# Kernel optimization log

Hardware: AMD Instinct MI355X
Metric: run time of the kernel (lower is better)

Reference implementation:

```python
import jax, jax.numpy as jnp
import numpy as np

B, L, D, H = 2, 2048, 1024, 16
HD = D // H


def setup_inputs() -> dict:
    key = jax.random.key(0)
    ks = jax.random.split(key, 8)
    x = jax.random.normal(ks[0], (B, L, D), dtype=jnp.float32)
    WQ = jax.random.normal(ks[1], (D, D), dtype=jnp.float32) * 0.02
    bQ = jnp.zeros((D,), dtype=jnp.float32)
    WK = jax.random.normal(ks[2], (D, D), dtype=jnp.float32) * 0.02
    bK = jnp.zeros((D,), dtype=jnp.float32)
    WV = jax.random.normal(ks[3], (D, D), dtype=jnp.float32) * 0.02
    bV = jnp.zeros((D,), dtype=jnp.float32)
    Wc = jax.random.normal(ks[4], (D, D), dtype=jnp.float32) * 0.02  # dense channel-mix matrix [d_out, d_in]
    return {"x": x, "WQ": WQ, "bQ": bQ, "WK": WK, "bK": bK, "WV": WV, "bV": bV, "Wc": Wc}


def reference(x, WQ, bQ, WK, bK, WV, bV, Wc):
    b, l, d = x.shape
    # --- TokenMixWeightGenerator (LOW_RANK): T = softmax(causal(Q K^T / sqrt(hd)))
    q = (x @ WQ.T + bQ).reshape(b, l, H, HD).transpose(0, 2, 1, 3)  # [B,H,L,hd]
    k = (x @ WK.T + bK).reshape(b, l, H, HD).transpose(0, 2, 1, 3)  # [B,H,L,hd]
    scores = jnp.einsum("bhid,bhjd->bhij", q, k) / jnp.sqrt(jnp.float32(HD))
    causal_mask = jnp.tril(jnp.ones((l, l), dtype=bool))  # keep j <= i
    scores = jnp.where(causal_mask, scores, -jnp.inf)
    T = jax.nn.softmax(scores, axis=-1)  # [B,H,L,L] explicit token-mix matrix
    # --- UnifiedFeaturizer (expansion=1): V reshaped per head
    v = (x @ WV.T + bV).reshape(b, l, H, HD).transpose(0, 2, 1, 3)  # [B,H,L,hd]
    # --- Y = C @ (T @ V)
    mixed = jnp.einsum("bhij,bhjd->bhid", T, v)  # [B,H,L,hd]
    mixed = mixed.transpose(0, 2, 1, 3).reshape(b, l, d)  # [B,L,D]
    y = mixed @ Wc.T  # channel mixing: output = input @ W.T
    return y
```

## Files before the change

kernel.cpp:

```cpp
#include <hip/hip_runtime.h>


typedef __bf16 bf16x8 __attribute__((ext_vector_type(8)));
typedef float f32x4 __attribute__((ext_vector_type(4)));
typedef unsigned short us4 __attribute__((ext_vector_type(4)));

#if defined(__has_builtin)
#if __has_builtin(__builtin_amdgcn_global_load_lds)
#define HAS_GLL 1
#endif
#endif
#ifndef HAS_GLL
#define HAS_GLL 0
#endif

__device__ __forceinline__ float bf2f(unsigned short u) {
    union { unsigned int i; float f; } v; v.i = ((unsigned int)u) << 16; return v.f;
}
__device__ __forceinline__ unsigned short f2bf(float f) {
    union { float f; unsigned int i; } v; v.f = f;
    unsigned int r = v.i + 0x7FFFu + ((v.i >> 16) & 1u);
    return (unsigned short)(r >> 16);
}
__device__ __forceinline__ unsigned short f2bf_fast(float f) {
    union { float f; unsigned int i; } v; v.f = f;
    return (unsigned short)((v.i + 0x8000u) >> 16);
}
__device__ __forceinline__ f32x4 mfma16(bf16x8 a, bf16x8 b, f32x4 c) {
    return __builtin_amdgcn_mfma_f32_16x16x32_bf16(a, b, c, 0, 0, 0);
}
__device__ __forceinline__ float clamp4(float v) {
    return fminf(fmaxf(v, -1e4f), 1e4f);
}
union U8 { unsigned short s[8]; bf16x8 v; };

#if HAS_GLL
__device__ __forceinline__ void gl_lds16(const unsigned short* g, unsigned short* l) {
    __builtin_amdgcn_global_load_lds(
        (const __attribute__((address_space(1))) void*)g,
        (__attribute__((address_space(3))) void*)l, 16, 0, 0);
}
#endif


__global__ __launch_bounds__(256) void convert_all(
    const float* __restrict__ x, const float* __restrict__ WQ,
    const float* __restrict__ WK, const float* __restrict__ WV,
    const float* __restrict__ Wc,
    unsigned short* __restrict__ xbf, unsigned short* __restrict__ wbf)
{
    size_t e = ((size_t)blockIdx.x * 256 + threadIdx.x) * 8;
    const float* src; unsigned short* dst; size_t off;
    if (e < 4194304) { src = x; dst = xbf; off = e; }
    else {
        size_t j = e - 4194304; int sel = (int)(j >> 20); off = j & 1048575;
        src = (sel == 0) ? WQ : (sel == 1) ? WK : (sel == 2) ? WV : Wc;
        dst = wbf + (size_t)sel * 1048576;
    }
    f32x4 a = *(const f32x4*)(src + off);
    f32x4 b = *(const f32x4*)(src + off + 4);
    U8 u;
    u.s[0] = f2bf(a[0]); u.s[1] = f2bf(a[1]); u.s[2] = f2bf(a[2]); u.s[3] = f2bf(a[3]);
    u.s[4] = f2bf(b[0]); u.s[5] = f2bf(b[1]); u.s[6] = f2bf(b[2]); u.s[7] = f2bf(b[3]);
    *(bf16x8*)(dst + off) = u.v;
}

__global__ __launch_bounds__(256) void gemm128(
    const unsigned short* __restrict__ A, const unsigned short* __restrict__ Wbase,
    const float* __restrict__ b0, const float* __restrict__ b1, const float* __restrict__ b2,
    void* __restrict__ d0, void* __restrict__ d1, void* __restrict__ d2, int modeBase)
{
    const int z = blockIdx.z;
    const unsigned short* W = Wbase + (size_t)z * 1048576;
    const float* bias = (z == 0) ? b0 : (z == 1) ? b1 : b2;
    void* dst = (z == 0) ? d0 : (z == 1) ? d1 : d2;
    const int mode = modeBase + z;

    __shared__ __align__(16) unsigned short At[128][32];
    __shared__ __align__(16) unsigned short Bt[128][32];

    const int mb = blockIdx.y * 128, nb = blockIdx.x * 128;
    const int tid = threadIdx.x, w = tid >> 6, lane = tid & 63;
    const int wr = w >> 1, wc = w & 1;
    const int col = lane & 15, quad = lane >> 4;

    f32x4 acc[4][4];
    for (int i = 0; i < 4; ++i) for (int j = 0; j < 4; ++j) acc[i][j] = (f32x4){0.f, 0.f, 0.f, 0.f};

#if HAS_GLL
    const unsigned short* ga = A + (size_t)(mb + w * 32 + (lane >> 2)) * 1024 + (lane & 3) * 8;
    const unsigned short* gw = W + (size_t)(nb + w * 32 + (lane >> 2)) * 1024 + (lane & 3) * 8;
    unsigned short* lA0 = &At[w * 32][0];
    unsigned short* lA1 = &At[w * 32 + 16][0];
    unsigned short* lB0 = &Bt[w * 32][0];
    unsigned short* lB1 = &Bt[w * 32 + 16][0];
#else
    const int srow = w * 32 + (lane >> 1);
    const int scol = (lane & 1) * 16;
    const unsigned short* Ab = A + (size_t)(mb + srow) * 1024 + scol;
    const unsigned short* Wb = W + (size_t)(nb + srow) * 1024 + scol;
#endif

    for (int kb = 0; kb < 1024; kb += 32) {
#if HAS_GLL
        gl_lds16(ga + kb, lA0);
        gl_lds16(ga + kb + 16 * 1024, lA1);
        gl_lds16(gw + kb, lB0);
        gl_lds16(gw + kb + 16 * 1024, lB1);
#else
        *(bf16x8*)&At[srow][scol]     = *(const bf16x8*)(Ab + kb);
        *(bf16x8*)&At[srow][scol + 8] = *(const bf16x8*)(Ab + kb + 8);
        *(bf16x8*)&Bt[srow][scol]     = *(const bf16x8*)(Wb + kb);
        *(bf16x8*)&Bt[srow][scol + 8] = *(const bf16x8*)(Wb + kb + 8);
#endif
        __syncthreads();
        bf16x8 a[4], b[4];
        for (int i = 0; i < 4; ++i) a[i] = *(const bf16x8*)&At[wr * 64 + i * 16 + col][quad * 8];
        for (int j = 0; j < 4; ++j) b[j] = *(const bf16x8*)&Bt[wc * 64 + j * 16 + col][quad * 8];
        for (int i = 0; i < 4; ++i)
            for (int j = 0; j < 4; ++j)
                acc[i][j] = mfma16(a[i], b[j], acc[i][j]);
        __syncthreads();
    }

    for (int i = 0; i < 4; ++i) {
        const int mbase = mb + wr * 64 + i * 16 + quad * 4;
        const int bb = mbase >> 11, l = mbase & 2047;
        for (int j = 0; j < 4; ++j) {
            const int n = nb + wc * 64 + j * 16 + col;
            const float bv = bias ? bias[n] : 0.f;
            if (mode == 3) {
                float* o = (float*)dst;
                for (int r = 0; r < 4; ++r)
                    o[(size_t)(mbase + r) * 1024 + n] = clamp4(acc[i][j][r] + bv);
            } else if (mode == 2) {
                const int h = n >> 6, hd = n & 63;
                us4 pk;
                for (int r = 0; r < 4; ++r) pk[r] = f2bf(clamp4(acc[i][j][r] + bv));
                *(us4*)((unsigned short*)dst + (size_t)(bb * 16 + h) * 131072
                        + (size_t)hd * 2048 + l) = pk;
            } else {
                const int h = n >> 6, hd = n & 63;
                unsigned short* o = (unsigned short*)dst + (size_t)(bb * 16 + h) * 131072
                                    + (size_t)l * 64 + hd;
                for (int r = 0; r < 4; ++r)
                    o[(size_t)r * 64] = f2bf(clamp4(acc[i][j][r] + bv));
            }
        }
    }
}

__device__ __forceinline__ void attn_tile_step(
    const unsigned short (*__restrict__ Kt)[72], const unsigned short (*__restrict__ Vt)[72],
    unsigned short (*__restrict__ Pw)[72],
    bf16x8 aq0, bf16x8 aq1, bf16x8 ones,
    f32x4* __restrict__ oacc, f32x4& lacc,
    bool diag, int col, int quad, int w)
{
    f32x4 s[4];
    for (int t = 0; t < 4; ++t) {
        bf16x8 bk0 = *(const bf16x8*)&Kt[t * 16 + col][quad * 8];
        bf16x8 bk1 = *(const bf16x8*)&Kt[t * 16 + col][32 + quad * 8];
        f32x4 z4 = (f32x4){0.f, 0.f, 0.f, 0.f};
        z4 = mfma16(aq0, bk0, z4);
        s[t] = mfma16(aq1, bk1, z4);
    }
    for (int t = 0; t < 4; ++t)
        for (int r = 0; r < 4; ++r) {
            float v = s[t][r] * 0.125f;
            if (diag && (t * 16 + col > w * 16 + quad * 4 + r)) v = -1e30f;
            v = fminf(v, 60.f);
            Pw[quad * 4 + r][t * 16 + col] = f2bf_fast(__expf(v));
        }
    bf16x8 ap0 = *(const bf16x8*)&Pw[col][quad * 8];
    bf16x8 ap1 = *(const bf16x8*)&Pw[col][32 + quad * 8];
    lacc = mfma16(ap0, ones, lacc);
    lacc = mfma16(ap1, ones, lacc);
    for (int nt = 0; nt < 4; ++nt) {
        bf16x8 bv0 = *(const bf16x8*)&Vt[nt * 16 + col][quad * 8];
        bf16x8 bv1 = *(const bf16x8*)&Vt[nt * 16 + col][32 + quad * 8];
        oacc[nt] = mfma16(ap0, bv0, oacc[nt]);
        oacc[nt] = mfma16(ap1, bv1, oacc[nt]);
    }
}

__device__ __forceinline__ void attn_write(
    unsigned short* __restrict__ mixed, int gb, int h, int q0, int col, int quad,
    const f32x4* __restrict__ oacc, f32x4 lacc)
{
    f32x4 inv;
    for (int r = 0; r < 4; ++r) inv[r] = 1.f / lacc[r];
    for (int nt = 0; nt < 4; ++nt)
        for (int r = 0; r < 4; ++r) {
            int qrow = q0 + quad * 4 + r;
            mixed[(size_t)(gb * 2048 + qrow) * 1024 + h * 64 + nt * 16 + col] =
                f2bf(clamp4(oacc[nt][r] * inv[r]));
        }
}

__global__ __launch_bounds__(256) void attn_pair(
    const unsigned short* __restrict__ Q, const unsigned short* __restrict__ K,
    const unsigned short* __restrict__ V, unsigned short* __restrict__ mixed)
{
    const int ca = blockIdx.x, cb = 31 - ca, bh = blockIdx.y;
    const int tid = threadIdx.x, w = tid >> 6, lane = tid & 63;
    const int col = lane & 15, quad = lane >> 4;

    __shared__ __align__(16) unsigned short Kt[64][72];
    __shared__ __align__(16) unsigned short Vt[64][72];
    __shared__ __align__(16) unsigned short Plds[4][16][72];

    const unsigned short* Qb = Q + (size_t)bh * 131072;
    const unsigned short* Kb = K + (size_t)bh * 131072;
    const unsigned short* Vb = V + (size_t)bh * 131072;

    const int qa0 = ca * 64 + w * 16, qb0 = cb * 64 + w * 16;
    bf16x8 aqa0 = *(const bf16x8*)(Qb + (size_t)(qa0 + col) * 64 + quad * 8);
    bf16x8 aqa1 = *(const bf16x8*)(Qb + (size_t)(qa0 + col) * 64 + 32 + quad * 8);
    bf16x8 aqb0 = *(const bf16x8*)(Qb + (size_t)(qb0 + col) * 64 + quad * 8);
    bf16x8 aqb1 = *(const bf16x8*)(Qb + (size_t)(qb0 + col) * 64 + 32 + quad * 8);

    U8 onesu;
    for (int i = 0; i < 8; ++i) onesu.s[i] = 0x3F80;
    const bf16x8 ones = onesu.v;

    f32x4 oa[4], ob[4];
    f32x4 la = (f32x4){0.f, 0.f, 0.f, 0.f}, lb = (f32x4){0.f, 0.f, 0.f, 0.f};
    for (int i = 0; i < 4; ++i) { oa[i] = la; ob[i] = la; }

    const int sr = tid >> 3, sc = (tid & 7) * 8;

    const unsigned short* kp = Kb + (size_t)sr * 64 + sc;
    const unsigned short* vp = Vb + (size_t)sr * 2048 + sc;
    bf16x8 pk0 = *(const bf16x8*)kp, pk1 = *(const bf16x8*)(kp + 32 * 64);
    bf16x8 pv0 = *(const bf16x8*)vp, pv1 = *(const bf16x8*)(vp + 32 * 2048);

    for (int kt = 0; kt <= cb; ++kt) {
        __syncthreads();
        *(bf16x8*)&Kt[sr][sc]      = pk0;
        *(bf16x8*)&Kt[sr + 32][sc] = pk1;
        *(bf16x8*)&Vt[sr][sc]      = pv0;
        *(bf16x8*)&Vt[sr + 32][sc] = pv1;
        __syncthreads();
        if (kt < cb) {
            const int kb2 = (kt + 1) * 64;
            const unsigned short* kp2 = Kb + (size_t)(kb2 + sr) * 64 + sc;
            const unsigned short* vp2 = Vb + (size_t)sr * 2048 + kb2 + sc;
            pk0 = *(const bf16x8*)kp2; pk1 = *(const bf16x8*)(kp2 + 32 * 64);
            pv0 = *(const bf16x8*)vp2; pv1 = *(const bf16x8*)(vp2 + 32 * 2048);
        }
        attn_tile_step(Kt, Vt, Plds[w], aqb0, aqb1, ones, ob, lb, kt == cb, col, quad, w);
        if (kt <= ca)
            attn_tile_step(Kt, Vt, Plds[w], aqa0, aqa1, ones, oa, la, kt == ca, col, quad, w);
    }

    const int gb = bh >> 4, h = bh & 15;
    attn_write(mixed, gb, h, qa0, col, quad, oa, la);
    attn_write(mixed, gb, h, qb0, col, quad, ob, lb);
}


__device__ __forceinline__ bf16x8 load8(const void* base, size_t eoff, int asF32) {
    if (asF32) {
        const float* p = (const float*)base + eoff;
        f32x4 a = *(const f32x4*)p;
        f32x4 b = *(const f32x4*)(p + 4);
        U8 u;
        u.s[0]=f2bf(a[0]); u.s[1]=f2bf(a[1]); u.s[2]=f2bf(a[2]); u.s[3]=f2bf(a[3]);
        u.s[4]=f2bf(b[0]); u.s[5]=f2bf(b[1]); u.s[6]=f2bf(b[2]); u.s[7]=f2bf(b[3]);
        return u.v;
    }
    return *(const bf16x8*)((const unsigned short*)base + eoff);
}

__global__ void dtype_probe(const unsigned short* __restrict__ x, int* __restrict__ flag) {
    if (threadIdx.x == 0) {
        int c = 0;
        for (int i = 0; i < 128; ++i) {
            int e = (x[2 * i] >> 7) & 0xFF;
            if (e >= 100 && e <= 135) ++c;
        }
        *flag = (c < 64) ? 1 : 0;
    }
}

__global__ __launch_bounds__(256) void gemm_bt(
    const void* __restrict__ Ap, const void* __restrict__ Wp,
    const void* __restrict__ biasp, void* __restrict__ dout,
    unsigned short* __restrict__ wsdst, const int* __restrict__ flag,
    long aOff, long outOff, int mode, int aFlagged)
{
    const int f32 = *flag;
    __shared__ __align__(16) unsigned short At[64][32];
    __shared__ __align__(16) unsigned short Bt[64][32];
    const int mb = blockIdx.y * 64, nb = blockIdx.x * 64;
    const int tid = threadIdx.x;
    const int w = tid >> 6, lane = tid & 63;
    const int wr = w >> 1, wc = w & 1;
    const int col = lane & 15, quad = lane >> 4;
    const int srow = tid >> 2, schunk = (tid & 3) * 8;
    const int aF = aFlagged && f32;

    f32x4 acc[2][2];
    for (int i = 0; i < 2; ++i) for (int j = 0; j < 2; ++j) acc[i][j] = (f32x4){0.f,0.f,0.f,0.f};

    const size_t aBase = (size_t)aOff + (size_t)(mb + srow) * 1024 + schunk;
    const size_t wBase = (size_t)(nb + srow) * 1024 + schunk;

    for (int kb = 0; kb < 1024; kb += 32) {
        *(bf16x8*)(&At[srow][schunk]) = load8(Ap, aBase + kb, aF);
        *(bf16x8*)(&Bt[srow][schunk]) = load8(Wp, wBase + kb, f32);
        __syncthreads();
        bf16x8 a0 = *(const bf16x8*)(&At[wr * 32 + col][quad * 8]);
        bf16x8 a1 = *(const bf16x8*)(&At[wr * 32 + 16 + col][quad * 8]);
        bf16x8 b0 = *(const bf16x8*)(&Bt[wc * 32 + col][quad * 8]);
        bf16x8 b1 = *(const bf16x8*)(&Bt[wc * 32 + 16 + col][quad * 8]);
        acc[0][0] = mfma16(a0, b0, acc[0][0]);
        acc[0][1] = mfma16(a0, b1, acc[0][1]);
        acc[1][0] = mfma16(a1, b0, acc[1][0]);
        acc[1][1] = mfma16(a1, b1, acc[1][1]);
        __syncthreads();
    }

    for (int mi = 0; mi < 2; ++mi) {
        for (int ni = 0; ni < 2; ++ni) {
            int n = nb + wc * 32 + ni * 16 + col;
            float bv = 0.f;
            if (biasp) bv = f32 ? ((const float*)biasp)[n] : bf2f(((const unsigned short*)biasp)[n]);
            for (int r = 0; r < 4; ++r) {
                int m = mb + wr * 32 + mi * 16 + quad * 4 + r;
                float v = clamp4(acc[mi][ni][r] + bv);
                if (mode == 3) {
                    size_t idx = (size_t)outOff + (size_t)m * 1024 + n;
                    if (f32) ((float*)dout)[idx] = v;
                    else     ((unsigned short*)dout)[idx] = f2bf(v);
                } else {
                    int h = n >> 6, hd = n & 63;
                    size_t idx = (mode == 2)
                        ? (size_t)h * 131072 + (size_t)hd * 2048 + m
                        : (size_t)h * 131072 + (size_t)m * 64 + hd;
                    unsigned short* dstp = (mode == 0)
                        ? (unsigned short*)dout + (f32 ? 4194304 : 2097152)
                        : wsdst;
                    dstp[idx] = f2bf(v);
                }
            }
        }
    }
}

__global__ __launch_bounds__(256) void attn_kernel(
    const void* __restrict__ dout, const unsigned short* __restrict__ Kw,
    const unsigned short* __restrict__ Vw, unsigned short* __restrict__ mixed,
    const int* __restrict__ flag)
{
    const int f32 = *flag;
    const int qtile = blockIdx.x;
    const int h = blockIdx.y;
    const int w = threadIdx.x >> 6, lane = threadIdx.x & 63;
    const int col = lane & 15, quad = lane >> 4;

    __shared__ __align__(16) unsigned short Plds[4][16][64];

    const unsigned short* Qs = (const unsigned short*)dout + (f32 ? 4194304 : 2097152);
    const unsigned short* Qb = Qs + (size_t)h * 131072;
    const unsigned short* Kb = Kw + (size_t)h * 131072;
    const unsigned short* Vb = Vw + (size_t)h * 131072;

    const int q0 = qtile * 64 + w * 16;
    bf16x8 aq0 = *(const bf16x8*)(Qb + (size_t)(q0 + col) * 64 + quad * 8);
    bf16x8 aq1 = *(const bf16x8*)(Qb + (size_t)(q0 + col) * 64 + 32 + quad * 8);

    float m_run[4] = {-1e30f, -1e30f, -1e30f, -1e30f};
    float l_run[4] = {0.f, 0.f, 0.f, 0.f};
    f32x4 oacc[4];
    for (int i = 0; i < 4; ++i) oacc[i] = (f32x4){0.f, 0.f, 0.f, 0.f};

    for (int kt = 0; kt <= qtile; ++kt) {
        const int kb = kt * 64;
        f32x4 s[4];
        for (int t = 0; t < 4; ++t) {
            s[t] = (f32x4){0.f, 0.f, 0.f, 0.f};
            bf16x8 bk0 = *(const bf16x8*)(Kb + (size_t)(kb + t * 16 + col) * 64 + quad * 8);
            bf16x8 bk1 = *(const bf16x8*)(Kb + (size_t)(kb + t * 16 + col) * 64 + 32 + quad * 8);
            s[t] = mfma16(aq0, bk0, s[t]);
            s[t] = mfma16(aq1, bk1, s[t]);
        }
        for (int t = 0; t < 4; ++t)
            for (int r = 0; r < 4; ++r) {
                float v = clamp4(s[t][r] * 0.125f);
                if (kt == qtile && (t * 16 + col > w * 16 + quad * 4 + r)) v = -1e30f;
                s[t][r] = v;
            }
        float mt[4];
        for (int r = 0; r < 4; ++r)
            mt[r] = fmaxf(fmaxf(s[0][r], s[1][r]), fmaxf(s[2][r], s[3][r]));
        for (int off = 1; off < 16; off <<= 1)
            for (int r = 0; r < 4; ++r)
                mt[r] = fmaxf(mt[r], __shfl_xor(mt[r], off, 64));
        float alpha[4], rs[4], p[4][4];
        for (int r = 0; r < 4; ++r) {
            float mn = fmaxf(m_run[r], mt[r]);
            alpha[r] = __expf(m_run[r] - mn);
            m_run[r] = mn;
        }
        for (int t = 0; t < 4; ++t)
            for (int r = 0; r < 4; ++r)
                p[t][r] = __expf(s[t][r] - m_run[r]);
        for (int r = 0; r < 4; ++r)
            rs[r] = (p[0][r] + p[1][r]) + (p[2][r] + p[3][r]);
        for (int off = 1; off < 16; off <<= 1)
            for (int r = 0; r < 4; ++r)
                rs[r] += __shfl_xor(rs[r], off, 64);
        for (int r = 0; r < 4; ++r)
            l_run[r] = l_run[r] * alpha[r] + rs[r];
        for (int nt = 0; nt < 4; ++nt)
            for (int r = 0; r < 4; ++r)
                oacc[nt][r] *= alpha[r];
        for (int t = 0; t < 4; ++t)
            for (int r = 0; r < 4; ++r)
                Plds[w][quad * 4 + r][t * 16 + col] = f2bf(p[t][r]);
        __syncthreads();
        bf16x8 ap0 = *(const bf16x8*)(&Plds[w][col][quad * 8]);
        bf16x8 ap1 = *(const bf16x8*)(&Plds[w][col][32 + quad * 8]);
        for (int nt = 0; nt < 4; ++nt) {
            bf16x8 bv0 = *(const bf16x8*)(Vb + (size_t)(nt * 16 + col) * 2048 + kb + quad * 8);
            bf16x8 bv1 = *(const bf16x8*)(Vb + (size_t)(nt * 16 + col) * 2048 + kb + 32 + quad * 8);
            oacc[nt] = mfma16(ap0, bv0, oacc[nt]);
            oacc[nt] = mfma16(ap1, bv1, oacc[nt]);
        }
        __syncthreads();
    }

    float inv[4];
    for (int r = 0; r < 4; ++r) inv[r] = 1.f / l_run[r];
    for (int nt = 0; nt < 4; ++nt)
        for (int r = 0; r < 4; ++r) {
            int qrow = q0 + quad * 4 + r;
            mixed[(size_t)qrow * 1024 + h * 64 + nt * 16 + col] = f2bf(clamp4(oacc[nt][r] * inv[r]));
        }
}


extern "C" void kernel_launch(void* const* d_in, const int* in_sizes, int n_in,
                              void* d_out, int out_size, void* d_ws, size_t ws_size,
                              hipStream_t stream) {
    (void)in_sizes; (void)n_in; (void)out_size;
    const void* x  = d_in[0];
    const void* WQ = d_in[1]; const void* bQ = d_in[2];
    const void* WK = d_in[3]; const void* bK = d_in[4];
    const void* WV = d_in[5]; const void* bV = d_in[6];
    const void* Wc = d_in[7];

    if (ws_size >= (size_t)32 * 1024 * 1024) {
        unsigned short* wbf   = (unsigned short*)d_ws;
        unsigned short* Kst   = wbf + 4194304;
        unsigned short* VTst  = Kst + 4194304;
        unsigned short* mixed = VTst + 4194304;
        unsigned short* xbf   = (unsigned short*)d_out;
        unsigned short* Qst   = xbf + 4194304;

        convert_all<<<4096, 256, 0, stream>>>(
            (const float*)x, (const float*)WQ, (const float*)WK,
            (const float*)WV, (const float*)Wc, xbf, wbf);

        gemm128<<<dim3(8, 32, 3), 256, 0, stream>>>(
            xbf, wbf, (const float*)bQ, (const float*)bK, (const float*)bV,
            Qst, Kst, VTst, 0);

        attn_pair<<<dim3(16, 32), 256, 0, stream>>>(Qst, Kst, VTst, mixed);

        gemm128<<<dim3(8, 32, 1), 256, 0, stream>>>(
            mixed, wbf + 3145728, nullptr, nullptr, nullptr,
            d_out, nullptr, nullptr, 3);
    } else {
        unsigned short* wsK = (unsigned short*)d_ws;
        unsigned short* wsV = wsK + 2097152;
        unsigned short* wsM = wsV + 2097152;
        int* flag = (int*)((char*)d_ws + 12 * 1024 * 1024);

        dtype_probe<<<1, 64, 0, stream>>>((const unsigned short*)x, flag);

        dim3 gg(16, 32), gb(256);
        for (int b = 0; b < 2; ++b) {
            long xo = (long)b * 2048 * 1024;
            gemm_bt<<<gg, gb, 0, stream>>>(x, WQ, bQ, d_out, nullptr, flag, xo, 0, 0, 1);
            gemm_bt<<<gg, gb, 0, stream>>>(x, WK, bK, d_out, wsK, flag, xo, 0, 1, 1);
            gemm_bt<<<gg, gb, 0, stream>>>(x, WV, bV, d_out, wsV, flag, xo, 0, 2, 1);
            attn_kernel<<<dim3(32, 16), 256, 0, stream>>>(d_out, wsK, wsV, wsM, flag);
            gemm_bt<<<gg, gb, 0, stream>>>(wsM, Wc, nullptr, d_out, nullptr, flag,
                                           0, (long)b * 2048 * 1024, 3, 0);
        }
    }
}
```

Before: 193.8 us.

## Double-buffer attention K/V tiles, widen GEMM k-step, fold softmax scale into Q

The attention kernel now double-buffers the K/V tiles in shared memory, so the next tile is written while the current one is used, with one barrier per iteration instead of two. The diagonal mask is made a template parameter, which removes the per-element branch on non-diagonal tiles. The 1/sqrt(hd)*log2(e) factor is folded into Q in the projection GEMM epilogue so the softmax can use the hardware exp2 directly, at the cost of a slightly different rounding and clamp. The GEMM K tile is doubled to 64, halving the number of barriers per output tile while doubling LDS use.

```diff
diff --git a/kernel.cpp b/kernel.cpp
--- a/kernel.cpp
+++ b/kernel.cpp
@@ -9,10 +9,18 @@
 #if __has_builtin(__builtin_amdgcn_global_load_lds)
 #define HAS_GLL 1
 #endif
+#if __has_builtin(__builtin_amdgcn_exp2f)
+#define EXP2(x) __builtin_amdgcn_exp2f(x)
+#endif
 #endif
 #ifndef HAS_GLL
 #define HAS_GLL 0
 #endif
+#ifndef EXP2
+#define EXP2(x) exp2f(x)
+#endif
+
+#define QSCALE 0.18033688f
 
 __device__ __forceinline__ float bf2f(unsigned short u) {
     union { unsigned int i; float f; } v; v.i = ((unsigned int)u) << 16; return v.f;
@@ -76,8 +84,8 @@
     void* dst = (z == 0) ? d0 : (z == 1) ? d1 : d2;
     const int mode = modeBase + z;
 
-    __shared__ __align__(16) unsigned short At[128][32];
-    __shared__ __align__(16) unsigned short Bt[128][32];
+    __shared__ __align__(16) unsigned short At[128][64];
+    __shared__ __align__(16) unsigned short Bt[128][64];
 
     const int mb = blockIdx.y * 128, nb = blockIdx.x * 128;
     const int tid = threadIdx.x, w = tid >> 6, lane = tid & 63;
@@ -88,41 +96,41 @@
     for (int i = 0; i < 4; ++i) for (int j = 0; j < 4; ++j) acc[i][j] = (f32x4){0.f, 0.f, 0.f, 0.f};
 
 #if HAS_GLL
-    const unsigned short* ga = A + (size_t)(mb + w * 32 + (lane >> 2)) * 1024 + (lane & 3) * 8;
-    const unsigned short* gw = W + (size_t)(nb + w * 32 + (lane >> 2)) * 1024 + (lane & 3) * 8;
-    unsigned short* lA0 = &At[w * 32][0];
-    unsigned short* lA1 = &At[w * 32 + 16][0];
-    unsigned short* lB0 = &Bt[w * 32][0];
-    unsigned short* lB1 = &Bt[w * 32 + 16][0];
+    const unsigned short* ga = A + (size_t)(mb + w * 32 + (lane >> 3)) * 1024 + (lane & 7) * 8;
+    const unsigned short* gw = W + (size_t)(nb + w * 32 + (lane >> 3)) * 1024 + (lane & 7) * 8;
 #else
-    const int srow = w * 32 + (lane >> 1);
-    const int scol = (lane & 1) * 16;
+    const int srow = tid >> 1, scol = (tid & 1) * 16;
     const unsigned short* Ab = A + (size_t)(mb + srow) * 1024 + scol;
     const unsigned short* Wb = W + (size_t)(nb + srow) * 1024 + scol;
 #endif
 
-    for (int kb = 0; kb < 1024; kb += 32) {
+    for (int kb = 0; kb < 1024; kb += 64) {
 #if HAS_GLL
-        gl_lds16(ga + kb, lA0);
-        gl_lds16(ga + kb + 16 * 1024, lA1);
-        gl_lds16(gw + kb, lB0);
-        gl_lds16(gw + kb + 16 * 1024, lB1);
+        for (int p = 0; p < 4; ++p) {
+            gl_lds16(ga + (size_t)p * 8 * 1024 + kb, &At[w * 32 + p * 8][0]);
+            gl_lds16(gw + (size_t)p * 8 * 1024 + kb, &Bt[w * 32 + p * 8][0]);
+        }
 #else
-        *(bf16x8*)&At[srow][scol]     = *(const bf16x8*)(Ab + kb);
-        *(bf16x8*)&At[srow][scol + 8] = *(const bf16x8*)(Ab + kb + 8);
-        *(bf16x8*)&Bt[srow][scol]     = *(const bf16x8*)(Wb + kb);
-        *(bf16x8*)&Bt[srow][scol + 8] = *(const bf16x8*)(Wb + kb + 8);
-#endif
-        __syncthreads();
-        bf16x8 a[4], b[4];
-        for (int i = 0; i < 4; ++i) a[i] = *(const bf16x8*)&At[wr * 64 + i * 16 + col][quad * 8];
-        for (int j = 0; j < 4; ++j) b[j] = *(const bf16x8*)&Bt[wc * 64 + j * 16 + col][quad * 8];
-        for (int i = 0; i < 4; ++i)
+        *(bf16x8*)&At[srow][scol]      = *(const bf16x8*)(Ab + kb);
+        *(bf16x8*)&At[srow][scol + 32] = *(const bf16x8*)(Ab + kb + 32);
+        *(bf16x8*)&Bt[srow][scol]      = *(const bf16x8*)(Wb + kb);
+        *(bf16x8*)&Bt[srow][scol + 32] = *(const bf16x8*)(Wb + kb + 32);
+#endif
+        __syncthreads();
+        for (int kk = 0; kk < 64; kk += 32) {
+            bf16x8 a[4], b[4];
+            for (int i = 0; i < 4; ++i)
+                a[i] = *(const bf16x8*)&At[wr * 64 + i * 16 + col][kk + quad * 8];
             for (int j = 0; j < 4; ++j)
-                acc[i][j] = mfma16(a[i], b[j], acc[i][j]);
-        __syncthreads();
-    }
-
+                b[j] = *(const bf16x8*)&Bt[wc * 64 + j * 16 + col][kk + quad * 8];
+            for (int i = 0; i < 4; ++i)
+                for (int j = 0; j < 4; ++j)
+                    acc[i][j] = mfma16(a[i], b[j], acc[i][j]);
+        }
+        __syncthreads();
+    }
+
+    const float oscale = (mode == 0) ? QSCALE : 1.f;
     for (int i = 0; i < 4; ++i) {
         const int mbase = mb + wr * 64 + i * 16 + quad * 4;
         const int bb = mbase >> 11, l = mbase & 2047;
@@ -144,18 +152,18 @@
                 unsigned short* o = (unsigned short*)dst + (size_t)(bb * 16 + h) * 131072
                                     + (size_t)l * 64 + hd;
                 for (int r = 0; r < 4; ++r)
-                    o[(size_t)r * 64] = f2bf(clamp4(acc[i][j][r] + bv));
+                    o[(size_t)r * 64] = f2bf(clamp4(acc[i][j][r] + bv) * oscale);
             }
         }
     }
 }
 
+template <bool DIAG>
 __device__ __forceinline__ void attn_tile_step(
     const unsigned short (*__restrict__ Kt)[72], const unsigned short (*__restrict__ Vt)[72],
     unsigned short (*__restrict__ Pw)[72],
     bf16x8 aq0, bf16x8 aq1, bf16x8 ones,
-    f32x4* __restrict__ oacc, f32x4& lacc,
-    bool diag, int col, int quad, int w)
+    f32x4* __restrict__ oacc, f32x4& lacc, int col, int quad, int w)
 {
     f32x4 s[4];
     for (int t = 0; t < 4; ++t) {
@@ -167,10 +175,10 @@
     }
     for (int t = 0; t < 4; ++t)
         for (int r = 0; r < 4; ++r) {
-            float v = s[t][r] * 0.125f;
-            if (diag && (t * 16 + col > w * 16 + quad * 4 + r)) v = -1e30f;
-            v = fminf(v, 60.f);
-            Pw[quad * 4 + r][t * 16 + col] = f2bf_fast(__expf(v));
+            float v = s[t][r];
+            if (DIAG && (t * 16 + col > w * 16 + quad * 4 + r)) v = -1e30f;
+            v = fminf(v, 100.f);
+            Pw[quad * 4 + r][t * 16 + col] = f2bf_fast(EXP2(v));
         }
     bf16x8 ap0 = *(const bf16x8*)&Pw[col][quad * 8];
     bf16x8 ap1 = *(const bf16x8*)&Pw[col][32 + quad * 8];
@@ -206,8 +214,8 @@
     const int tid = threadIdx.x, w = tid >> 6, lane = tid & 63;
     const int col = lane & 15, quad = lane >> 4;
 
-    __shared__ __align__(16) unsigned short Kt[64][72];
-    __shared__ __align__(16) unsigned short Vt[64][72];
+    __shared__ __align__(16) unsigned short Kt[2][64][72];
+    __shared__ __align__(16) unsigned short Vt[2][64][72];
     __shared__ __align__(16) unsigned short Plds[4][16][72];
 
     const unsigned short* Qb = Q + (size_t)bh * 131072;
@@ -229,29 +237,42 @@
     for (int i = 0; i < 4; ++i) { oa[i] = la; ob[i] = la; }
 
     const int sr = tid >> 3, sc = (tid & 7) * 8;
-
-    const unsigned short* kp = Kb + (size_t)sr * 64 + sc;
-    const unsigned short* vp = Vb + (size_t)sr * 2048 + sc;
-    bf16x8 pk0 = *(const bf16x8*)kp, pk1 = *(const bf16x8*)(kp + 32 * 64);
-    bf16x8 pv0 = *(const bf16x8*)vp, pv1 = *(const bf16x8*)(vp + 32 * 2048);
+    const unsigned short* kp0 = Kb + (size_t)sr * 64 + sc;
+    const unsigned short* vp0 = Vb + (size_t)sr * 2048 + sc;
+
+    {
+        bf16x8 k0 = *(const bf16x8*)kp0, k1 = *(const bf16x8*)(kp0 + 32 * 64);
+        bf16x8 v0 = *(const bf16x8*)vp0, v1 = *(const bf16x8*)(vp0 + 32 * 2048);
+        *(bf16x8*)&Kt[0][sr][sc] = k0; *(bf16x8*)&Kt[0][sr + 32][sc] = k1;
+        *(bf16x8*)&Vt[0][sr][sc] = v0; *(bf16x8*)&Vt[0][sr + 32][sc] = v1;
+    }
+    __syncthreads();
 
     for (int kt = 0; kt <= cb; ++kt) {
-        __syncthreads();
-        *(bf16x8*)&Kt[sr][sc]      = pk0;
-        *(bf16x8*)&Kt[sr + 32][sc] = pk1;
-        *(bf16x8*)&Vt[sr][sc]      = pv0;
-        *(bf16x8*)&Vt[sr + 32][sc] = pv1;
-        __syncthreads();
-        if (kt < cb) {
+        const int cur = kt & 1;
+        bf16x8 pk0, pk1, pv0, pv1;
+        const bool more = (kt < cb);
+        if (more) {
             const int kb2 = (kt + 1) * 64;
-            const unsigned short* kp2 = Kb + (size_t)(kb2 + sr) * 64 + sc;
-            const unsigned short* vp2 = Vb + (size_t)sr * 2048 + kb2 + sc;
+            const unsigned short* kp2 = kp0 + (size_t)kb2 * 64;
+            const unsigned short* vp2 = vp0 + kb2;
             pk0 = *(const bf16x8*)kp2; pk1 = *(const bf16x8*)(kp2 + 32 * 64);
             pv0 = *(const bf16x8*)vp2; pv1 = *(const bf16x8*)(vp2 + 32 * 2048);
         }
-        attn_tile_step(Kt, Vt, Plds[w], aqb0, aqb1, ones, ob, lb, kt == cb, col, quad, w);
-        if (kt <= ca)
-            attn_tile_step(Kt, Vt, Plds[w], aqa0, aqa1, ones, oa, la, kt == ca, col, quad, w);
+        if (kt == cb)
+            attn_tile_step<true >(Kt[cur], Vt[cur], Plds[w], aqb0, aqb1, ones, ob, lb, col, quad, w);
+        else
+            attn_tile_step<false>(Kt[cur], Vt[cur], Plds[w], aqb0, aqb1, ones, ob, lb, col, quad, w);
+        if (kt < ca)
+            attn_tile_step<false>(Kt[cur], Vt[cur], Plds[w], aqa0, aqa1, ones, oa, la, col, quad, w);
+        else if (kt == ca)
+            attn_tile_step<true >(Kt[cur], Vt[cur], Plds[w], aqa0, aqa1, ones, oa, la, col, quad, w);
+        if (more) {
+            const int nxt = cur ^ 1;
+            *(bf16x8*)&Kt[nxt][sr][sc] = pk0; *(bf16x8*)&Kt[nxt][sr + 32][sc] = pk1;
+            *(bf16x8*)&Vt[nxt][sr][sc] = pv0; *(bf16x8*)&Vt[nxt][sr + 32][sc] = pv1;
+        }
+        __syncthreads();
     }
 
     const int gb = bh >> 4, h = bh & 15;
```

After: 361.9 us. +86.8%, slower.
